# Optimization experiments

Measured on AMD Instinct MI355X. Metric: run time of the kernel, lower is better.

Reference implementation:

```python
import jax, jax.numpy as jnp
import numpy as np

LMAX, MMAX = 4, 2
L = (LMAX + 1) ** 2  # 25 full SH coefficients
_midx = np.concatenate([l * l + l + np.arange(-min(l, MMAX), min(l, MMAX) + 1) for l in range(LMAX + 1)])
M = len(_midx)  # 19 m-restricted coefficients (|m|<=mmax)
_l_of = np.concatenate([np.full(2 * l + 1, l) for l in range(LMAX + 1)])
MIDX = jnp.asarray(_midx)
L_OF = jnp.asarray(_l_of)
LMAP = jnp.asarray((_l_of[:, None] == np.arange(LMAX + 1)[None, :]).astype(np.float32))  # [L, lmax+1]
COUNTS = jnp.asarray((2 * np.arange(LMAX + 1) + 1).astype(np.float32))
AVG_DEGREE = 23.395238876342773
AVG_NUM_NODES = 77.81317
N_NODES, N_EDGES, N_GRAPH = 2500, 50000, 16
C, H, A, VC, FF, NB, NL = 128, 8, 64, 16, 128, 600, 4
MAX_R = 12.0

def rms_norm_sh(x, scale):
    # per-degree-l RMS norm with learned per-(l, channel) scale; x [N,L,C]
    ms = jnp.einsum('nlc,lk->nk', x * x, LMAP) / (COUNTS * x.shape[-1])
    inv = jax.lax.rsqrt(ms + 1e-8)[:, L_OF]  # [N,L]
    return x * inv[..., None] * scale[L_OF][None]

def seg_softmax(logits, seg, n):
    m = jax.ops.segment_max(logits, seg, num_segments=n)
    e = jnp.exp(logits - m[seg])
    s = jax.ops.segment_sum(e, seg, num_segments=n)
    return e / (s[seg] + 1e-9)

def _forward(edge_distance, sphere_emb, W_e1, W_e2, W_deg, norm_scale, norm_scale2,
             Wq, Wk, alpha_vec, Wv, W_rad, Wo, W1, W2, norm_scale_final, W_ef1, W_ef2,
             atomic_numbers, edge_index, batch):
    src, tgt = edge_index[0], edge_index[1]
    # GaussianSmearing(0, max_radius, 600, basis_width_scalar=2.0)
    offset = jnp.linspace(0.0, MAX_R, NB)
    coeff = -0.5 / (2.0 * (MAX_R / (NB - 1))) ** 2
    smear = jnp.exp(coeff * (edge_distance[:, None] - offset[None, :]) ** 2)  # [E,NB]
    efeat = jax.nn.silu(jax.nn.silu(smear @ W_e1) @ W_e2)  # shared radial edge features [E,C]
    # sphere embedding into l=0 coefficient
    x = jnp.zeros((N_NODES, L, C), edge_distance.dtype)
    x = x.at[:, 0, :].set(sphere_emb[atomic_numbers])
    # edge degree embedding: per-edge coefficients scattered to target nodes
    deg = (efeat @ W_deg).reshape(N_EDGES, M, C)
    x = x.at[:, MIDX, :].add(jax.ops.segment_sum(deg, tgt, num_segments=N_NODES) / AVG_DEGREE)
    for i in range(NL):
        # --- SO2 equivariant graph attention ---
        xn = rms_norm_sh(x, norm_scale[i])
        s = xn[:, 0, :]  # invariant (l=0) features [N,C]
        q = (s @ Wq[i]).reshape(N_NODES, H, A)[tgt]
        k = (s @ Wk[i]).reshape(N_NODES, H, A)[src]
        logits = jnp.einsum('eha,ha->eh', jax.nn.silu(q + k), alpha_vec[i]) / np.sqrt(A).astype(np.float32)
        attn = seg_softmax(logits, tgt, N_NODES)  # [E,H]
        rad = jax.nn.silu(efeat @ W_rad[i])  # per-edge per-coefficient radial gate [E,M]
        xm = xn[:, MIDX, :][src] * rad[..., None]  # gather m-restricted coeffs [E,M,C]
        v = jnp.einsum('emc,cd->emd', xm, Wv[i]).reshape(N_EDGES, M, H, VC)
        msg = (v * attn[:, None, :, None]).reshape(N_EDGES, M, H * VC)
        out = jnp.einsum('emd,dc->emc', msg, Wo[i])
        x = x.at[:, MIDX, :].add(jax.ops.segment_sum(out, tgt, num_segments=N_NODES))
        # --- FFN with separable S2 (scalar-gated) activation ---
        xn = rms_norm_sh(x, norm_scale2[i])
        h = jnp.einsum('nlc,cf->nlf', xn, W1[i])
        h = h * jax.nn.silu(h[:, :1, :])
        x = x + jnp.einsum('nlf,fc->nlc', h, W2[i])
    # energy head
    xn = rms_norm_sh(x, norm_scale_final)
    h = jnp.einsum('nlc,cf->nlf', xn, W_ef1)
    h = h * jax.nn.silu(h[:, :1, :])
    node_e = jnp.einsum('nlf,fo->nlo', h, W_ef2)[:, 0, 0]  # l=0 scalar per node
    return jax.ops.segment_sum(node_e, batch, num_segments=N_GRAPH) / AVG_NUM_NODES

def setup_inputs() -> dict:
    key = jax.random.key(0)
    ks = jax.random.split(key, 24)
    rn = lambda k, shp, fan: jax.random.normal(k, shp, jnp.float32) / np.sqrt(fan).astype(np.float32)
    inp = {}
    inp['atomic_numbers'] = jax.random.randint(ks[0], (N_NODES,), 0, 90)
    inp['edge_index'] = jax.random.randint(ks[1], (2, N_EDGES), 0, N_NODES)
    inp['edge_distance'] = jax.random.uniform(ks[2], (N_EDGES,), jnp.float32) * MAX_R
    inp['batch'] = jnp.sort(jax.random.randint(ks[3], (N_NODES,), 0, N_GRAPH))
    inp['sphere_emb'] = rn(ks[4], (90, C), 1)
    inp['W_e1'] = rn(ks[5], (NB, C), NB)
    inp['W_e2'] = rn(ks[6], (C, C), C)
    inp['W_deg'] = rn(ks[7], (C, M * C), C)
    inp['norm_scale'] = jnp.ones((NL, LMAX + 1, C), jnp.float32)
    inp['norm_scale2'] = jnp.ones((NL, LMAX + 1, C), jnp.float32)
    inp['Wq'] = rn(ks[8], (NL, C, H * A), C)
    inp['Wk'] = rn(ks[9], (NL, C, H * A), C)
    inp['alpha_vec'] = rn(ks[10], (NL, H, A), A)
    inp['Wv'] = rn(ks[11], (NL, C, H * VC), C)
    inp['W_rad'] = rn(ks[12], (NL, C, M), C)
    inp['Wo'] = rn(ks[13], (NL, H * VC, C), H * VC)
    inp['W1'] = rn(ks[14], (NL, C, FF), C)
    inp['W2'] = rn(ks[15], (NL, FF, C), FF)
    inp['norm_scale_final'] = jnp.ones((LMAX + 1, C), jnp.float32)
    inp['W_ef1'] = rn(ks[16], (C, FF), C)
    inp['W_ef2'] = rn(ks[17], (FF, 1), FF)
    return inp

def reference(atomic_numbers, edge_index, edge_distance, batch, sphere_emb, W_e1, W_e2, W_deg,
              norm_scale, norm_scale2, Wq, Wk, alpha_vec, Wv, W_rad, Wo, W1, W2,
              norm_scale_final, W_ef1, W_ef2):
    return _forward(edge_distance, sphere_emb, W_e1, W_e2, W_deg, norm_scale, norm_scale2,
                    Wq, Wk, alpha_vec, Wv, W_rad, Wo, W1, W2, norm_scale_final, W_ef1, W_ef2,
                    atomic_numbers, edge_index, batch)
```

## Files before the change

kernel.cpp:

```cpp
#include <hip/hip_runtime.h>
#include <hip/hip_bf16.h>

#define N_NODES 2500
#define N_EDGES 50000
#define C 128
#define MC 19
#define RSTR 20
#define NL 4
#define NB 600
#define GW 12
#define NTAP (2*GW+1)
#define NBUK 4
#define BUKW 625
#define N4 (N_NODES*NBUK)
#define ASTR 136
#define MSTR 132
#define MAXE 96
#define EB 64

typedef float floatx2 __attribute__((ext_vector_type(2)));
typedef short bf16x8 __attribute__((ext_vector_type(8)));
typedef float f32x4 __attribute__((ext_vector_type(4)));

__device__ __forceinline__ float silu(float v){ return v / (1.f + expf(-v)); }
__device__ __forceinline__ int l_of_m(int m){
  return (m==0)?0 : (m<4)?1 : (m<9)?2 : (m<14)?3 : 4;
}
__device__ __forceinline__ unsigned pack2(float a, float b){
  __hip_bfloat162 h2;
  h2.x = __float2bfloat16(a);
  h2.y = __float2bfloat16(b);
  return *(unsigned*)&h2;
}
__device__ __forceinline__ unsigned short bf16of(float v){
  __hip_bfloat16 h = __float2bfloat16(v);
  return *(unsigned short*)&h;
}
__device__ __forceinline__ float2 bf2f2(unsigned u){
  float2 r;
  r.x = __uint_as_float(u << 16);
  r.y = __uint_as_float(u & 0xffff0000u);
  return r;
}
__device__ __forceinline__ bf16x8 packbf8(float4 a, float4 b){
  union { unsigned u[4]; bf16x8 v; } r;
  r.u[0] = pack2(a.x, a.y); r.u[1] = pack2(a.z, a.w);
  r.u[2] = pack2(b.x, b.y); r.u[3] = pack2(b.z, b.w);
  return r.v;
}
__device__ __forceinline__ unsigned short packfp8(float a, float b){
  float ac = fminf(fmaxf(a, -448.f), 448.f);
  float bc = fminf(fmaxf(b, -448.f), 448.f);
  return (unsigned short)((unsigned)__builtin_amdgcn_cvt_pk_fp8_f32(ac, bc, 0, false) & 0xffffu);
}

__global__ __launch_bounds__(256) void k_packall(
    const float* __restrict__ We2, const float* __restrict__ Wv, const float* __restrict__ Wo,
    const float* __restrict__ W1, const float* __restrict__ W2,
    const float* __restrict__ Wq, const float* __restrict__ Wk,
    unsigned short* we2t, unsigned short* wvt, unsigned short* wot,
    unsigned short* w1t, unsigned short* w2t, unsigned short* wqt, unsigned short* wkt){
  unsigned id = blockIdx.x*256 + threadIdx.x;
  const unsigned PERL = 98304u;
  if (id < 8192u){
    unsigned f = id & 127u, cp = id >> 7;
    *(unsigned*)&we2t[f*C + 2*cp] = pack2(We2[(2*cp)*C + f], We2[(2*cp+1)*C + f]);
    return;
  }
  unsigned rem = id - 8192u;
  unsigned layer = rem / PERL;
  if (layer >= 4u) return;
// ... 170 lines not shown
        const float* __restrict__ emb, const int* __restrict__ anum, float* __restrict__ x){
  __shared__ __align__(16) float efT[C][16];
  int t = threadIdx.x;
  int n0 = blockIdx.x*16;
  int grp = blockIdx.y;
  for (int q=t; q<16*C; q+=256){
    int cc=q>>4, nd=q&15;
    int n=n0+nd;
    efT[cc][nd] = (n<N_NODES)? efsumT[(size_t)cc*N_NODES + n] : 0.f;
  }
  __syncthreads();
  const float inv_avg = 1.0f/23.395238876342773f;
  int o = grp*512 + t*2;
  if (o < MC*C){
    float a0[16], a1[16];
    #pragma unroll
    for (int i=0;i<16;i++){ a0[i]=0.f; a1[i]=0.f; }
    for (int cc=0; cc<C; ++cc){
      float2 w = *(const float2*)&Wdeg[(size_t)cc*(MC*C)+o];
      float4 e0 = *(const float4*)&efT[cc][0];
      float4 e1 = *(const float4*)&efT[cc][4];
      float4 e2 = *(const float4*)&efT[cc][8];
      float4 e3 = *(const float4*)&efT[cc][12];
      a0[0]+=e0.x*w.x; a1[0]+=e0.x*w.y;
      a0[1]+=e0.y*w.x; a1[1]+=e0.y*w.y;
      a0[2]+=e0.z*w.x; a1[2]+=e0.z*w.y;
      a0[3]+=e0.w*w.x; a1[3]+=e0.w*w.y;
      a0[4]+=e1.x*w.x; a1[4]+=e1.x*w.y;
      a0[5]+=e1.y*w.x; a1[5]+=e1.y*w.y;
      a0[6]+=e1.z*w.x; a1[6]+=e1.z*w.y;
      a0[7]+=e1.w*w.x; a1[7]+=e1.w*w.y;
      a0[8]+=e2.x*w.x; a1[8]+=e2.x*w.y;
      a0[9]+=e2.y*w.x; a1[9]+=e2.y*w.y;
      a0[10]+=e2.z*w.x; a1[10]+=e2.z*w.y;
      a0[11]+=e2.w*w.x; a1[11]+=e2.w*w.y;
      a0[12]+=e3.x*w.x; a1[12]+=e3.x*w.y;
      a0[13]+=e3.y*w.x; a1[13]+=e3.y*w.y;
      a0[14]+=e3.z*w.x; a1[14]+=e3.z*w.y;
      a0[15]+=e3.w*w.x; a1[15]+=e3.w*w.y;
    }
    #pragma unroll
    for (int nd=0; nd<16; ++nd){
      int n = n0+nd;
      if (n < N_NODES){
        float v0 = a0[nd]*inv_avg, v1 = a1[nd]*inv_avg;
        if (o < C){ int an=anum[n]; v0 += emb[an*C+o]; v1 += emb[an*C+o+1]; }
        float2 st; st.x=v0; st.y=v1;
        *(float2*)&x[(size_t)n*MC*C + o] = st;
      }
    }
  }
}

__global__ __launch_bounds__(256) void k_qk(const float* __restrict__ x, const float* __restrict__ scale0,
        const unsigned short* __restrict__ wqt, const unsigned short* __restrict__ wkt,
        unsigned short* __restrict__ qb, unsigned short* __restrict__ kb){
  __shared__ __align__(16) float sn[32][132];
  __shared__ float ps[32][8];
  __shared__ float invs[32];
  __shared__ __align__(16) unsigned short A16[32*ASTR];
  int t = threadIdx.x;
  int n0 = blockIdx.x*32;
  int grp = blockIdx.y;
  const unsigned short* WTg = (grp < 4) ? wqt : wkt;
  int cb = (grp & 3)*128;
  unsigned short* outb = (grp < 4) ? qb : kb;
  {
    int nd = t>>3, seg = t&7;
    int n = n0+nd;
    float ss = 0.f;
    if (n < N_NODES){
      const float* xr = &x[(size_t)n*MC*C];
      #pragma unroll
      for (int i=0;i<16;i++){
        int c = seg*16+i;
        float v = xr[c];
        ss += v*v;
        sn[nd][c] = v*scale0[c];
      }
    } else {
      #pragma unroll
      for (int i=0;i<16;i++) sn[nd][seg*16+i] = 0.f;
    }
    ps[nd][seg] = ss;
  }
  __syncthreads();
  if (t < 32){
    float s = 0.f;
    #pragma unroll
    for (int i=0;i<8;i++) s += ps[t][i];
    invs[t] = 1.0f/sqrtf(s*(1.0f/128.f) + 1e-8f);
  }
  __syncthreads();
  for (int q=t; q<32*64; q+=256){
    int r = q>>6, c2 = (q&63)*2;
    float inv = invs[r];
    *(unsigned*)&A16[r*ASTR + c2] = pack2(sn[r][c2]*inv, sn[r][c2+1]*inv);
  }
  __syncthreads();
  int w = t>>6, lane = t&63;
  int lr = lane & 15, lg = lane >> 4;
  int colb = 32*w;
  f32x4 acc[2][2];
  #pragma unroll
  for (int rt=0;rt<2;rt++)
    #pragma unroll
    for (int ci=0;ci<2;ci++){ acc[rt][ci][0]=0.f; acc[rt][ci][1]=0.f; acc[rt][ci][2]=0.f; acc[rt][ci][3]=0.f; }
  #pragma unroll
  for (int ks=0; ks<4; ++ks){
    int k0 = ks*32 + lg*8;
    const unsigned short* Ab = &A16[lr*ASTR + k0];
    bf16x8 a0 = *(const bf16x8*)(Ab);
    bf16x8 a1 = *(const bf16x8*)(Ab + 16*ASTR);
    const unsigned short* Bb = &WTg[(size_t)(cb + colb + lr)*C + k0];
    bf16x8 b0 = *(const bf16x8*)(Bb);
    bf16x8 b1 = *(const bf16x8*)(Bb + 16*C);
    acc[0][0] = __builtin_amdgcn_mfma_f32_16x16x32_bf16(a0, b0, acc[0][0], 0, 0, 0);
    acc[1][0] = __builtin_amdgcn_mfma_f32_16x16x32_bf16(a1, b0, acc[1][0], 0, 0, 0);
    acc[0][1] = __builtin_amdgcn_mfma_f32_16x16x32_bf16(a0, b1, acc[0][1], 0, 0, 0);
    acc[1][1] = __builtin_amdgcn_mfma_f32_16x16x32_bf16(a1, b1, acc[1][1], 0, 0, 0);
  }
  #pragma unroll
  for (int rt=0;rt<2;rt++){
    #pragma unroll
    for (int ci=0;ci<2;ci++){
      int col = colb + 16*ci + lr;
      #pragma unroll
      for (int q=0;q<4;q++){
        int r = 16*rt + lg*4 + q;
        int n = n0 + r;
        if (n < N_NODES)
          outb[(size_t)n*512 + cb + col] = bf16of(acc[rt][ci][q]);
      }
    }
  }
}

__global__ __launch_bounds__(256) void k_nodeA(const float* __restrict__ x, const float* __restrict__ scale,
        const unsigned short* __restrict__ wvt, unsigned char* __restrict__ V){
  __shared__ __align__(16) unsigned short A16[80*ASTR];
  int t = threadIdx.x;
  int n0 = blockIdx.x*4;
  int w = t>>6, lane = t&63;
  int lr = lane & 15, lg = lane >> 4;
  {
    int n = n0 + w;
    float2 xv[MC];
    float pl[5]={0.f,0.f,0.f,0.f,0.f};
    #pragma unroll
    for (int m=0;m<MC;m++){
      float2 v = *(const float2*)&x[(size_t)n*MC*C + m*C + lane*2];
      xv[m]=v;
      pl[l_of_m(m)] += v.x*v.x + v.y*v.y;
    }
    #pragma unroll
    for (int l=0;l<5;l++){
      float r = pl[l];
      #pragma unroll
      for (int d=32; d>0; d>>=1) r += __shfl_xor(r, d, 64);
      pl[l]=r;
    }
    const float dens[5] = {128.f,384.f,640.f,896.f,1152.f};
    float inv[5];
    #pragma unroll
    for (int l=0;l<5;l++) inv[l] = 1.0f/sqrtf(pl[l]/dens[l] + 1e-8f);
    #pragma unroll
    for (int m=0;m<MC;m++){
      int l = l_of_m(m);
      float2 sc = *(const float2*)&scale[l*C + lane*2];
      float a = xv[m].x*inv[l]*sc.x, b = xv[m].y*inv[l]*sc.y;
      *(unsigned*)&A16[(w*MC + m)*ASTR + lane*2] = pack2(a, b);
    }
  }
  for (int q=t; q<272; q+=256)
    ((unsigned*)A16)[(76*ASTR)/2 + q] = 0u;
  __syncthreads();
  int colb = 32*w;
  f32x4 acc[5][2];
  #pragma unroll
  for (int rt=0;rt<5;rt++)
    #pragma unroll
    for (int ci=0;ci<2;ci++){ acc[rt][ci][0]=0.f; acc[rt][ci][1]=0.f; acc[rt][ci][2]=0.f; acc[rt][ci][3]=0.f; }
  #pragma unroll
  for (int ks=0; ks<4; ++ks){
    int k0 = ks*32 + lg*8;
    const unsigned short* Ab = &A16[lr*ASTR + k0];
    bf16x8 a0 = *(const bf16x8*)(Ab);
    bf16x8 a1 = *(const bf16x8*)(Ab + 16*ASTR);
    bf16x8 a2 = *(const bf16x8*)(Ab + 32*ASTR);
    bf16x8 a3 = *(const bf16x8*)(Ab + 48*ASTR);
    bf16x8 a4 = *(const bf16x8*)(Ab + 64*ASTR);
    const unsigned short* Bb = &wvt[(colb + lr)*C + k0];
    bf16x8 b0 = *(const bf16x8*)(Bb);
    bf16x8 b1 = *(const bf16x8*)(Bb + 16*C);
    acc[0][0] = __builtin_amdgcn_mfma_f32_16x16x32_bf16(a0, b0, acc[0][0], 0, 0, 0);
    acc[1][0] = __builtin_amdgcn_mfma_f32_16x16x32_bf16(a1, b0, acc[1][0], 0, 0, 0);
    acc[2][0] = __builtin_amdgcn_mfma_f32_16x16x32_bf16(a2, b0, acc[2][0], 0, 0, 0);
    acc[3][0] = __builtin_amdgcn_mfma_f32_16x16x32_bf16(a3, b0, acc[3][0], 0, 0, 0);
    acc[4][0] = __builtin_amdgcn_mfma_f32_16x16x32_bf16(a4, b0, acc[4][0], 0, 0, 0);
    acc[0][1] = __builtin_amdgcn_mfma_f32_16x16x32_bf16(a0, b1, acc[0][1], 0, 0, 0);
    acc[1][1] = __builtin_amdgcn_mfma_f32_16x16x32_bf16(a1, b1, acc[1][1], 0, 0, 0);
    acc[2][1] = __builtin_amdgcn_mfma_f32_16x16x32_bf16(a2, b1, acc[2][1], 0, 0, 0);
    acc[3][1] = __builtin_amdgcn_mfma_f32_16x16x32_bf16(a3, b1, acc[3][1], 0, 0, 0);
    acc[4][1] = __builtin_amdgcn_mfma_f32_16x16x32_bf16(a4, b1, acc[4][1], 0, 0, 0);
  }
  __syncthreads();
  #pragma unroll
  for (int rt=0;rt<5;rt++){
    #pragma unroll
    for (int ci=0;ci<2;ci++){
      int col = colb + 16*ci + lr;
      #pragma unroll
      for (int q=0;q<4;q++){
        int r = 16*rt + lg*4 + q;
        A16[r*ASTR + col] = bf16of(acc[rt][ci][q]);
      }
    }
  }
  __syncthreads();
  for (int q=t; q<76*64; q+=256){
    int r = q>>6;
    int c2 = (q&63)*2;
    unsigned u = *(unsigned*)&A16[r*ASTR + c2];
    float2 f = bf2f2(u);
    *(unsigned short*)&V[((size_t)(n0*MC + r))*C + c2] = packfp8(f.x, f.y);
  }
}

__global__ __launch_bounds__(256) void k_attn(const unsigned short* __restrict__ qb,
        const unsigned short* __restrict__ kb, const float* __restrict__ alpha,
        const int* __restrict__ rowptr, const int2* __restrict__ epair, float* __restrict__ attnb){
  __shared__ float lw[4][MAXE][8];
  __shared__ int eid[4][MAXE];
  int t = threadIdx.x;
  int w = t>>6, lane = t&63;
  int n = blockIdx.x*4 + w;
  float al[8];
  {
    float4 a0 = *(const float4*)&alpha[lane*8];
    float4 a1 = *(const float4*)&alpha[lane*8+4];
    al[0]=a0.x; al[1]=a0.y; al[2]=a0.z; al[3]=a0.w;
    al[4]=a1.x; al[5]=a1.y; al[6]=a1.z; al[7]=a1.w;
  }
  float qf[8];
  {
    int4 qv = *(const int4*)&qb[(size_t)n*512 + lane*8];
    unsigned qu[4] = {(unsigned)qv.x,(unsigned)qv.y,(unsigned)qv.z,(unsigned)qv.w};
    #pragma unroll
    for (int j=0;j<4;j++){
      float2 q2 = bf2f2(qu[j]);
      qf[2*j] = q2.x; qf[2*j+1] = q2.y;
    }
  }
  int beg = rowptr[n*NBUK], end = rowptr[n*NBUK+NBUK];
  int cnt = end - beg; if (cnt > MAXE) cnt = MAXE;
  int i = 0;
  for (; i+2 <= cnt; i += 2){
    int2 p0 = epair[beg+i];
    int2 p1 = epair[beg+i+1];
    int4 kv0 = *(const int4*)&kb[(size_t)p0.y*512 + lane*8];
    int4 kv1 = *(const int4*)&kb[(size_t)p1.y*512 + lane*8];
    unsigned ku0[4] = {(unsigned)kv0.x,(unsigned)kv0.y,(unsigned)kv0.z,(unsigned)kv0.w};
    unsigned ku1[4] = {(unsigned)kv1.x,(unsigned)kv1.y,(unsigned)kv1.z,(unsigned)kv1.w};
    float acc0 = 0.f, acc1 = 0.f;
    #pragma unroll
    for (int j=0;j<4;j++){
      float2 k0 = bf2f2(ku0[j]);
      float2 k1 = bf2f2(ku1[j]);
      acc0 += silu(qf[2*j]+k0.x)*al[2*j] + silu(qf[2*j+1]+k0.y)*al[2*j+1];
      acc1 += silu(qf[2*j]+k1.x)*al[2*j] + silu(qf[2*j+1]+k1.y)*al[2*j+1];
    }
    #pragma unroll
    for (int d=1; d<8; d<<=1){
      acc0 += __shfl_down(acc0, d, 64);
      acc1 += __shfl_down(acc1, d, 64);
    }
    if ((lane&7)==0){
      lw[w][i][lane>>3]   = acc0 * 0.125f;
      lw[w][i+1][lane>>3] = acc1 * 0.125f;
    }
    if (lane==0){ eid[w][i] = p0.x; eid[w][i+1] = p1.x; }
  }
  for (; i < cnt; ++i){
    int2 p0 = epair[beg+i];
    int4 kv0 = *(const int4*)&kb[(size_t)p0.y*512 + lane*8];
    unsigned ku0[4] = {(unsigned)kv0.x,(unsigned)kv0.y,(unsigned)kv0.z,(unsigned)kv0.w};
    float acc0 = 0.f;
    #pragma unroll
    for (int j=0;j<4;j++){
      float2 k0 = bf2f2(ku0[j]);
      acc0 += silu(qf[2*j]+k0.x)*al[2*j] + silu(qf[2*j+1]+k0.y)*al[2*j+1];
    }
    #pragma unroll
    for (int d=1; d<8; d<<=1) acc0 += __shfl_down(acc0, d, 64);
    if ((lane&7)==0) lw[w][i][lane>>3] = acc0 * 0.125f;
    if (lane==0) eid[w][i] = p0.x;
  }
  __syncthreads();
  int h = lane & 7, ec = lane >> 3;
  float mx = -1e30f;
  for (int q=ec; q<cnt; q+=8) mx = fmaxf(mx, lw[w][q][h]);
  #pragma unroll
  for (int dd=8; dd<64; dd<<=1) mx = fmaxf(mx, __shfl_xor(mx, dd, 64));
  float sum = 0.f;
  for (int q=ec; q<cnt; q+=8) sum += expf(lw[w][q][h] - mx);
  #pragma unroll
  for (int dd=8; dd<64; dd<<=1) sum += __shfl_xor(sum, dd, 64);
  float inv = 1.0f/(sum + 1e-9f);
  for (int q=ec; q<cnt; q+=8)
    attnb[eid[w][q]*8 + h] = expf(lw[w][q][h] - mx) * inv;
}

__global__ __launch_bounds__(256) void k_rad(const float* __restrict__ efeat, const float* __restrict__ Wrad,
                                             float* __restrict__ radb){
  __shared__ __align__(16) unsigned short A16[EB*ASTR];
  __shared__ __align__(16) unsigned short WT[32*ASTR];
  int t = threadIdx.x;
  int e0 = blockIdx.x*EB;
  for (int q=t; q<EB*64; q+=256){
    int r = q>>6, c2 = (q&63)*2;
    int e = e0 + r;
    float2 f2;
    if (e < N_EDGES) f2 = *(const float2*)&efeat[(size_t)e*C + c2];
    else { f2.x=0.f; f2.y=0.f; }
    *(unsigned*)&A16[r*ASTR + c2] = pack2(f2.x, f2.y);
  }
  for (int q=t; q<32*64; q+=256){
    int m = q>>6, c2 = (q&63)*2;
    float w0 = (m < MC) ? Wrad[(size_t)c2*MC + m] : 0.f;
    float w1 = (m < MC) ? Wrad[(size_t)(c2+1)*MC + m] : 0.f;
    *(unsigned*)&WT[m*ASTR + c2] = pack2(w0, w1);
  }
  __syncthreads();
  int w = t>>6, lane = t&63;
  int lr = lane & 15, lg = lane >> 4;
  f32x4 acc[2];
  acc[0][0]=0.f; acc[0][1]=0.f; acc[0][2]=0.f; acc[0][3]=0.f;
  acc[1][0]=0.f; acc[1][1]=0.f; acc[1][2]=0.f; acc[1][3]=0.f;
  #pragma unroll
  for (int ks=0; ks<4; ++ks){
    int k0 = ks*32 + lg*8;
    bf16x8 a  = *(const bf16x8*)&A16[(16*w + lr)*ASTR + k0];
    bf16x8 b0 = *(const bf16x8*)&WT[lr*ASTR + k0];
    bf16x8 b1 = *(const bf16x8*)&WT[(16+lr)*ASTR + k0];
    acc[0] = __builtin_amdgcn_mfma_f32_16x16x32_bf16(a, b0, acc[0], 0, 0, 0);
    acc[1] = __builtin_amdgcn_mfma_f32_16x16x32_bf16(a, b1, acc[1], 0, 0, 0);
  }
  #pragma unroll
  for (int ci=0;ci<2;ci++){
    int m = 16*ci + lr;
    #pragma unroll
    for (int q=0;q<4;q++){
      int r = 16*w + lg*4 + q;
      int e = e0 + r;
      if (m < MC && e < N_EDGES)
        radb[(size_t)e*RSTR + m] = silu(acc[ci][q]);
    }
  }
}

#define CONS1(vv, ar)  { \
    floatx2 g0 = __builtin_amdgcn_cvt_pk_f32_fp8((vv).x, false); \
    floatx2 g1 = __builtin_amdgcn_cvt_pk_f32_fp8((vv).x, true);  \
    floatx2 g2 = __builtin_amdgcn_cvt_pk_f32_fp8((vv).y, false); \
    floatx2 g3 = __builtin_amdgcn_cvt_pk_f32_fp8((vv).y, true);  \
    acc1[0] += (ar)*g0[0]; acc1[1] += (ar)*g0[1]; \
    acc1[2] += (ar)*g1[0]; acc1[3] += (ar)*g1[1]; \
    acc1[4] += (ar)*g2[0]; acc1[5] += (ar)*g2[1]; \
    acc1[6] += (ar)*g3[0]; acc1[7] += (ar)*g3[1]; }
#define CONS2(vv, ar)  { \
    floatx2 g0 = __builtin_amdgcn_cvt_pk_f32_fp8((vv).x, false); \
    floatx2 g1 = __builtin_amdgcn_cvt_pk_f32_fp8((vv).x, true);  \
    floatx2 g2 = __builtin_amdgcn_cvt_pk_f32_fp8((vv).y, false); \
    floatx2 g3 = __builtin_amdgcn_cvt_pk_f32_fp8((vv).y, true);  \
    acc2[0] += (ar)*g0[0]; acc2[1] += (ar)*g0[1]; \
    acc2[2] += (ar)*g1[0]; acc2[3] += (ar)*g1[1]; \
    acc2[4] += (ar)*g2[0]; acc2[5] += (ar)*g2[1]; \
    acc2[6] += (ar)*g3[0]; acc2[7] += (ar)*g3[1]; }
__global__ __launch_bounds__(256, 4) void k_e1(const unsigned char* __restrict__ V, const float* __restrict__ radb,
        const float* __restrict__ attnb, const unsigned short* __restrict__ wot,
        const int* __restrict__ rowptr, const int2* __restrict__ epair,
        float* __restrict__ x){
  __shared__ __align__(16) float msum[32*MSTR];
  int n = blockIdx.x;
  int t = threadIdx.x;
  int w = t>>6, lane = t&63;
  for (int q=t; q<13*MSTR; q+=256) msum[19*MSTR + q] = 0.f;
  int chunk = lane & 15;
  int g = lane >> 4;
  int m1 = w*5 + g;
  int c1 = chunk*8;
  int h1 = chunk>>1;
  int m2 = w*5 + 4;
  bool has2 = (w < 3) && (lane < 16);
  int voff1 = m1*C + c1;
  int voff2 = m2*C + lane*8;
  int h2 = lane>>1;
  float acc1[8], acc2[8];
  #pragma unroll
  for (int j=0;j<8;j++){ acc1[j]=0.f; acc2[j]=0.f; }
  int beg = rowptr[n*NBUK], end = rowptr[n*NBUK+NBUK];
  int idx = beg;
  for (; idx+4 <= end; idx += 4){
    int2 p0 = epair[idx];
    int2 p1 = epair[idx+1];
    int2 p2 = epair[idx+2];
    int2 p3 = epair[idx+3];
    const unsigned char* vb0 = V + (size_t)p0.y*(MC*C);
    const unsigned char* vb1 = V + (size_t)p1.y*(MC*C);
// ... 281 lines not shown
  const float* emb   = (const float*)d_in[4];
  const float* We1   = (const float*)d_in[5];
  const float* We2   = (const float*)d_in[6];
  const float* Wdeg  = (const float*)d_in[7];
  const float* ns1   = (const float*)d_in[8];
  const float* ns2   = (const float*)d_in[9];
  const float* Wq    = (const float*)d_in[10];
  const float* Wk    = (const float*)d_in[11];
  const float* alpha = (const float*)d_in[12];
  const float* Wv    = (const float*)d_in[13];
  const float* Wrad  = (const float*)d_in[14];
  const float* Wo    = (const float*)d_in[15];
  const float* W1    = (const float*)d_in[16];
  const float* W2    = (const float*)d_in[17];
  const float* nsf   = (const float*)d_in[18];
  const float* Wef1  = (const float*)d_in[19];
  const float* Wef2  = (const float*)d_in[20];
  float* out = (float*)d_out;

  const int* srcarr = eidx;
  const int* tgtarr = eidx + N_EDGES;

  char* wsb = (char*)d_ws;
  float* efeat = (float*)wsb;  wsb += (size_t)N_EDGES*C*4;
  float* efsumT= (float*)wsb;  wsb += (size_t)N_NODES*C*4;
  float* x     = (float*)wsb;  wsb += (size_t)N_NODES*MC*C*4;
  unsigned char* Vb = (unsigned char*)wsb; wsb += (size_t)N_NODES*MC*C;
  unsigned short* qb = (unsigned short*)wsb; wsb += (size_t)N_NODES*512*2;
  unsigned short* kb = (unsigned short*)wsb; wsb += (size_t)N_NODES*512*2;
  float* attnb = (float*)wsb;  wsb += (size_t)N_EDGES*8*4;
  float* radb  = (float*)wsb;  wsb += (size_t)N_EDGES*RSTR*4;
  int* deg     = (int*)wsb;    wsb += (size_t)N4*4;
  int* rowptr  = (int*)wsb;    wsb += (size_t)(N4+1)*4;
  int* cursor  = (int*)wsb;    wsb += (size_t)N4*4;
  int* elist   = (int*)wsb;    wsb += (size_t)N_EDGES*4;
  int2* epair  = (int2*)wsb;   wsb += (size_t)N_EDGES*8;
  unsigned short* we2t = (unsigned short*)wsb; wsb += (size_t)16384*2;
  unsigned short* wvt  = (unsigned short*)wsb; wsb += (size_t)4*16384*2;
  unsigned short* wot  = (unsigned short*)wsb; wsb += (size_t)4*16384*2;
  unsigned short* w1t  = (unsigned short*)wsb; wsb += (size_t)4*16384*2;
  unsigned short* w2t  = (unsigned short*)wsb; wsb += (size_t)4*16384*2;
  unsigned short* wqt  = (unsigned short*)wsb; wsb += (size_t)4*65536*2;
  unsigned short* wkt  = (unsigned short*)wsb; wsb += (size_t)4*65536*2;

  (void)hipMemsetAsync(deg, 0, N4*4, stream);
  (void)hipMemsetAsync(cursor, 0, N4*4, stream);
  (void)hipMemsetAsync(d_out, 0, (size_t)out_size*sizeof(float), stream);

  k_packall<<<1568, 256, 0, stream>>>(We2, Wv, Wo, W1, W2, Wq, Wk,
                                      we2t, wvt, wot, w1t, w2t, wqt, wkt);
  k_count<<<(N_EDGES+255)/256, 256, 0, stream>>>(tgtarr, srcarr, deg);
  k_scan<<<1, 1024, 0, stream>>>(deg, rowptr);
  k_fill<<<(N_EDGES+255)/256, 256, 0, stream>>>(tgtarr, srcarr, rowptr, cursor, elist, epair);
  k_efeat<<<(N_EDGES+EB-1)/EB, 256, 0, stream>>>(dist, We1, we2t, efeat);
  k_efsum<<<N_NODES, 128, 0, stream>>>(efeat, rowptr, elist, efsumT);
  k_deginit<<<dim3((N_NODES+15)/16, 5), 256, 0, stream>>>(efsumT, Wdeg, emb, anum, x);

  for (int i=0;i<NL;i++){
    k_nodeA<<<N_NODES/4, 256, 0, stream>>>(x, ns1 + i*5*C, wvt + (size_t)i*16384, Vb);
    k_qk<<<dim3((N_NODES+31)/32, 8), 256, 0, stream>>>(x, ns1 + i*5*C,
                                                       wqt + (size_t)i*65536, wkt + (size_t)i*65536,
                                                       qb, kb);
    k_attn<<<N_NODES/4, 256, 0, stream>>>(qb, kb, alpha + i*512, rowptr, epair, attnb);
    k_rad<<<(N_EDGES+EB-1)/EB, 256, 0, stream>>>(efeat, Wrad + i*C*MC, radb);
    k_e1<<<N_NODES, 256, 0, stream>>>(Vb, radb, attnb, wot + (size_t)i*16384,
                                      rowptr, epair, x);
    k_nodeB<<<N_NODES/2/2, 256, 0, stream>>>(x, ns2 + i*5*C, w1t + (size_t)i*16384, w2t + (size_t)i*16384);
  }
  k_final<<<N_NODES, 128, 0, stream>>>(x, nsf, Wef1, Wef2, batch, out);
}
```

Baseline: 753.0 us.

## Merge independent per-layer kernels into horizontally fused launches

Within each layer, the value-projection kernel and the Q/K projection kernel now run as one launch, with block index deciding which branch runs, and the shared memory is carved from one byte buffer. The attention-softmax kernel and the radial-weight kernel are combined the same way. This removes two launches per layer and lets independent work fill the GPU at the same time, at the cost of the larger shared memory footprint and register pressure of the heavier branch applying to every block. It also narrows the Gaussian tap window constant GW from 12 to 10, which changes how many smearing taps are kept.

```diff
diff --git a/kernel.cpp b/kernel.cpp
--- a/kernel.cpp
+++ b/kernel.cpp
@@ -8,7 +8,7 @@
 #define RSTR 20
 #define NL 4
 #define NB 600
-#define GW 12
+#define GW 10
 #define NTAP (2*GW+1)
 #define NBUK 4
 #define BUKW 625
@@ -17,6 +17,8 @@
 #define MSTR 132
 #define MAXE 96
 #define EB 64
+#define NQKB ((N_NODES+31)/32)
+#define NRADB ((N_EDGES+EB-1)/EB)
 
 typedef float floatx2 __attribute__((ext_vector_type(2)));
 typedef short bf16x8 __attribute__((ext_vector_type(8)));
@@ -293,309 +295,307 @@
   }
 }
 
-__global__ __launch_bounds__(256) void k_qk(const float* __restrict__ x, const float* __restrict__ scale0,
-        const unsigned short* __restrict__ wqt, const unsigned short* __restrict__ wkt,
-        unsigned short* __restrict__ qb, unsigned short* __restrict__ kb){
-  __shared__ __align__(16) float sn[32][132];
-  __shared__ float ps[32][8];
-  __shared__ float invs[32];
-  __shared__ __align__(16) unsigned short A16[32*ASTR];
+__global__ __launch_bounds__(256) void k_nAqk(const float* __restrict__ x, const float* __restrict__ scale0,
+        const unsigned short* __restrict__ wvt, const unsigned short* __restrict__ wqt,
+        const unsigned short* __restrict__ wkt,
+        unsigned char* __restrict__ V, unsigned short* __restrict__ qb, unsigned short* __restrict__ kb){
+  __shared__ __align__(16) char smem[26880];
   int t = threadIdx.x;
-  int n0 = blockIdx.x*32;
-  int grp = blockIdx.y;
-  const unsigned short* WTg = (grp < 4) ? wqt : wkt;
-  int cb = (grp & 3)*128;
-  unsigned short* outb = (grp < 4) ? qb : kb;
-  {
-    int nd = t>>3, seg = t&7;
-    int n = n0+nd;
-    float ss = 0.f;
-    if (n < N_NODES){
-      const float* xr = &x[(size_t)n*MC*C];
-      #pragma unroll
-      for (int i=0;i<16;i++){
-        int c = seg*16+i;
-        float v = xr[c];
-        ss += v*v;
-        sn[nd][c] = v*scale0[c];
-      }
-    } else {
-      #pragma unroll
-      for (int i=0;i<16;i++) sn[nd][seg*16+i] = 0.f;
-    }
-    ps[nd][seg] = ss;
-  }
-  __syncthreads();
-  if (t < 32){
-    float s = 0.f;
-    #pragma unroll
-    for (int i=0;i<8;i++) s += ps[t][i];
-    invs[t] = 1.0f/sqrtf(s*(1.0f/128.f) + 1e-8f);
-  }
-  __syncthreads();
-  for (int q=t; q<32*64; q+=256){
-    int r = q>>6, c2 = (q&63)*2;
-    float inv = invs[r];
-    *(unsigned*)&A16[r*ASTR + c2] = pack2(sn[r][c2]*inv, sn[r][c2+1]*inv);
-  }
-  __syncthreads();
   int w = t>>6, lane = t&63;
   int lr = lane & 15, lg = lane >> 4;
-  int colb = 32*w;
-  f32x4 acc[2][2];
-  #pragma unroll
-  for (int rt=0;rt<2;rt++)
-    #pragma unroll
-    for (int ci=0;ci<2;ci++){ acc[rt][ci][0]=0.f; acc[rt][ci][1]=0.f; acc[rt][ci][2]=0.f; acc[rt][ci][3]=0.f; }
-  #pragma unroll
-  for (int ks=0; ks<4; ++ks){
-    int k0 = ks*32 + lg*8;
-    const unsigned short* Ab = &A16[lr*ASTR + k0];
-    bf16x8 a0 = *(const bf16x8*)(Ab);
-    bf16x8 a1 = *(const bf16x8*)(Ab + 16*ASTR);
-    const unsigned short* Bb = &WTg[(size_t)(cb + colb + lr)*C + k0];
-    bf16x8 b0 = *(const bf16x8*)(Bb);
-    bf16x8 b1 = *(const bf16x8*)(Bb + 16*C);
-    acc[0][0] = __builtin_amdgcn_mfma_f32_16x16x32_bf16(a0, b0, acc[0][0], 0, 0, 0);
-    acc[1][0] = __builtin_amdgcn_mfma_f32_16x16x32_bf16(a1, b0, acc[1][0], 0, 0, 0);
-    acc[0][1] = __builtin_amdgcn_mfma_f32_16x16x32_bf16(a0, b1, acc[0][1], 0, 0, 0);
-    acc[1][1] = __builtin_amdgcn_mfma_f32_16x16x32_bf16(a1, b1, acc[1][1], 0, 0, 0);
-  }
-  #pragma unroll
-  for (int rt=0;rt<2;rt++){
-    #pragma unroll
-    for (int ci=0;ci<2;ci++){
-      int col = colb + 16*ci + lr;
-      #pragma unroll
-      for (int q=0;q<4;q++){
-        int r = 16*rt + lg*4 + q;
-        int n = n0 + r;
-        if (n < N_NODES)
-          outb[(size_t)n*512 + cb + col] = bf16of(acc[rt][ci][q]);
-      }
-    }
-  }
-}
-
-__global__ __launch_bounds__(256) void k_nodeA(const float* __restrict__ x, const float* __restrict__ scale,
-        const unsigned short* __restrict__ wvt, unsigned char* __restrict__ V){
-  __shared__ __align__(16) unsigned short A16[80*ASTR];
-  int t = threadIdx.x;
-  int n0 = blockIdx.x*4;
-  int w = t>>6, lane = t&63;
-  int lr = lane & 15, lg = lane >> 4;
-  {
-    int n = n0 + w;
-    float2 xv[MC];
-    float pl[5]={0.f,0.f,0.f,0.f,0.f};
-    #pragma unroll
-    for (int m=0;m<MC;m++){
-      float2 v = *(const float2*)&x[(size_t)n*MC*C + m*C + lane*2];
-      xv[m]=v;
-      pl[l_of_m(m)] += v.x*v.x + v.y*v.y;
-    }
-    #pragma unroll
-    for (int l=0;l<5;l++){
-      float r = pl[l];
-      #pragma unroll
-      for (int d=32; d>0; d>>=1) r += __shfl_xor(r, d, 64);
-      pl[l]=r;
-    }
-    const float dens[5] = {128.f,384.f,640.f,896.f,1152.f};
-    float inv[5];
-    #pragma unroll
-    for (int l=0;l<5;l++) inv[l] = 1.0f/sqrtf(pl[l]/dens[l] + 1e-8f);
-    #pragma unroll
-    for (int m=0;m<MC;m++){
-      int l = l_of_m(m);
-      float2 sc = *(const float2*)&scale[l*C + lane*2];
-      float a = xv[m].x*inv[l]*sc.x, b = xv[m].y*inv[l]*sc.y;
-      *(unsigned*)&A16[(w*MC + m)*ASTR + lane*2] = pack2(a, b);
-    }
-  }
-  for (int q=t; q<272; q+=256)
-    ((unsigned*)A16)[(76*ASTR)/2 + q] = 0u;
-  __syncthreads();
-  int colb = 32*w;
-  f32x4 acc[5][2];
-  #pragma unroll
-  for (int rt=0;rt<5;rt++)
-    #pragma unroll
-    for (int ci=0;ci<2;ci++){ acc[rt][ci][0]=0.f; acc[rt][ci][1]=0.f; acc[rt][ci][2]=0.f; acc[rt][ci][3]=0.f; }
-  #pragma unroll
-  for (int ks=0; ks<4; ++ks){
-    int k0 = ks*32 + lg*8;
-    const unsigned short* Ab = &A16[lr*ASTR + k0];
-    bf16x8 a0 = *(const bf16x8*)(Ab);
-    bf16x8 a1 = *(const bf16x8*)(Ab + 16*ASTR);
-    bf16x8 a2 = *(const bf16x8*)(Ab + 32*ASTR);
-    bf16x8 a3 = *(const bf16x8*)(Ab + 48*ASTR);
-    bf16x8 a4 = *(const bf16x8*)(Ab + 64*ASTR);
-    const unsigned short* Bb = &wvt[(colb + lr)*C + k0];
-    bf16x8 b0 = *(const bf16x8*)(Bb);
-    bf16x8 b1 = *(const bf16x8*)(Bb + 16*C);
-    acc[0][0] = __builtin_amdgcn_mfma_f32_16x16x32_bf16(a0, b0, acc[0][0], 0, 0, 0);
-    acc[1][0] = __builtin_amdgcn_mfma_f32_16x16x32_bf16(a1, b0, acc[1][0], 0, 0, 0);
-    acc[2][0] = __builtin_amdgcn_mfma_f32_16x16x32_bf16(a2, b0, acc[2][0], 0, 0, 0);
-    acc[3][0] = __builtin_amdgcn_mfma_f32_16x16x32_bf16(a3, b0, acc[3][0], 0, 0, 0);
-    acc[4][0] = __builtin_amdgcn_mfma_f32_16x16x32_bf16(a4, b0, acc[4][0], 0, 0, 0);
-    acc[0][1] = __builtin_amdgcn_mfma_f32_16x16x32_bf16(a0, b1, acc[0][1], 0, 0, 0);
-    acc[1][1] = __builtin_amdgcn_mfma_f32_16x16x32_bf16(a1, b1, acc[1][1], 0, 0, 0);
-    acc[2][1] = __builtin_amdgcn_mfma_f32_16x16x32_bf16(a2, b1, acc[2][1], 0, 0, 0);
-    acc[3][1] = __builtin_amdgcn_mfma_f32_16x16x32_bf16(a3, b1, acc[3][1], 0, 0, 0);
-    acc[4][1] = __builtin_amdgcn_mfma_f32_16x16x32_bf16(a4, b1, acc[4][1], 0, 0, 0);
-  }
-  __syncthreads();
-  #pragma unroll
-  for (int rt=0;rt<5;rt++){
-    #pragma unroll
-    for (int ci=0;ci<2;ci++){
-      int col = colb + 16*ci + lr;
-      #pragma unroll
-      for (int q=0;q<4;q++){
-        int r = 16*rt + lg*4 + q;
-        A16[r*ASTR + col] = bf16of(acc[rt][ci][q]);
-      }
-    }
-  }
-  __syncthreads();
-  for (int q=t; q<76*64; q+=256){
-    int r = q>>6;
-    int c2 = (q&63)*2;
-    unsigned u = *(unsigned*)&A16[r*ASTR + c2];
-    float2 f = bf2f2(u);
-    *(unsigned short*)&V[((size_t)(n0*MC + r))*C + c2] = packfp8(f.x, f.y);
-  }
-}
-
-__global__ __launch_bounds__(256) void k_attn(const unsigned short* __restrict__ qb,
+  if (blockIdx.x < (unsigned)(N_NODES/4)){
+    unsigned short* A16 = (unsigned short*)smem;
+    int n0 = blockIdx.x*4;
+    {
+      int n = n0 + w;
+      float2 xv[MC];
+      float pl[5]={0.f,0.f,0.f,0.f,0.f};
+      #pragma unroll
+      for (int m=0;m<MC;m++){
+        float2 v = *(const float2*)&x[(size_t)n*MC*C + m*C + lane*2];
+        xv[m]=v;
+        pl[l_of_m(m)] += v.x*v.x + v.y*v.y;
+      }
+      #pragma unroll
+      for (int l=0;l<5;l++){
+        float r = pl[l];
+        #pragma unroll
+        for (int d=32; d>0; d>>=1) r += __shfl_xor(r, d, 64);
+        pl[l]=r;
+      }
+      const float dens[5] = {128.f,384.f,640.f,896.f,1152.f};
+      float inv[5];
+      #pragma unroll
+      for (int l=0;l<5;l++) inv[l] = 1.0f/sqrtf(pl[l]/dens[l] + 1e-8f);
+      #pragma unroll
+      for (int m=0;m<MC;m++){
+        int l = l_of_m(m);
+        float2 sc = *(const float2*)&scale0[l*C + lane*2];
+        float a = xv[m].x*inv[l]*sc.x, b = xv[m].y*inv[l]*sc.y;
+        *(unsigned*)&A16[(w*MC + m)*ASTR + lane*2] = pack2(a, b);
+      }
+    }
+    for (int q=t; q<272; q+=256)
+      ((unsigned*)A16)[(76*ASTR)/2 + q] = 0u;
+    __syncthreads();
+    int colb = 32*w;
+    f32x4 acc[5][2];
+    #pragma unroll
+    for (int rt=0;rt<5;rt++)
+      #pragma unroll
+      for (int ci=0;ci<2;ci++){ acc[rt][ci][0]=0.f; acc[rt][ci][1]=0.f; acc[rt][ci][2]=0.f; acc[rt][ci][3]=0.f; }
+    #pragma unroll
+    for (int ks=0; ks<4; ++ks){
+      int k0 = ks*32 + lg*8;
+      const unsigned short* Ab = &A16[lr*ASTR + k0];
+      bf16x8 a0 = *(const bf16x8*)(Ab);
+      bf16x8 a1 = *(const bf16x8*)(Ab + 16*ASTR);
+      bf16x8 a2 = *(const bf16x8*)(Ab + 32*ASTR);
+      bf16x8 a3 = *(const bf16x8*)(Ab + 48*ASTR);
+      bf16x8 a4 = *(const bf16x8*)(Ab + 64*ASTR);
+      const unsigned short* Bb = &wvt[(colb + lr)*C + k0];
+      bf16x8 b0 = *(const bf16x8*)(Bb);
+      bf16x8 b1 = *(const bf16x8*)(Bb + 16*C);
+      acc[0][0] = __builtin_amdgcn_mfma_f32_16x16x32_bf16(a0, b0, acc[0][0], 0, 0, 0);
+      acc[1][0] = __builtin_amdgcn_mfma_f32_16x16x32_bf16(a1, b0, acc[1][0], 0, 0, 0);
+      acc[2][0] = __builtin_amdgcn_mfma_f32_16x16x32_bf16(a2, b0, acc[2][0], 0, 0, 0);
+      acc[3][0] = __builtin_amdgcn_mfma_f32_16x16x32_bf16(a3, b0, acc[3][0], 0, 0, 0);
+      acc[4][0] = __builtin_amdgcn_mfma_f32_16x16x32_bf16(a4, b0, acc[4][0], 0, 0, 0);
+      acc[0][1] = __builtin_amdgcn_mfma_f32_16x16x32_bf16(a0, b1, acc[0][1], 0, 0, 0);
+      acc[1][1] = __builtin_amdgcn_mfma_f32_16x16x32_bf16(a1, b1, acc[1][1], 0, 0, 0);
+      acc[2][1] = __builtin_amdgcn_mfma_f32_16x16x32_bf16(a2, b1, acc[2][1], 0, 0, 0);
+      acc[3][1] = __builtin_amdgcn_mfma_f32_16x16x32_bf16(a3, b1, acc[3][1], 0, 0, 0);
+      acc[4][1] = __builtin_amdgcn_mfma_f32_16x16x32_bf16(a4, b1, acc[4][1], 0, 0, 0);
+    }
+    __syncthreads();
+    #pragma unroll
+    for (int rt=0;rt<5;rt++){
+      #pragma unroll
+      for (int ci=0;ci<2;ci++){
+        int col = colb + 16*ci + lr;
+        #pragma unroll
+        for (int q=0;q<4;q++){
+          int r = 16*rt + lg*4 + q;
+          A16[r*ASTR + col] = bf16of(acc[rt][ci][q]);
+        }
+      }
+    }
+    __syncthreads();
+    for (int q=t; q<76*64; q+=256){
+      int r = q>>6;
+      int c2 = (q&63)*2;
+      unsigned u = *(unsigned*)&A16[r*ASTR + c2];
+      float2 f = bf2f2(u);
+      *(unsigned short*)&V[((size_t)(n0*MC + r))*C + c2] = packfp8(f.x, f.y);
+    }
+  } else {
+    int qq = blockIdx.x - N_NODES/4;
+    int grp = qq / NQKB;
+    int n0 = (qq - grp*NQKB)*32;
+    float (*sn)[132] = (float(*)[132])smem;
+    float (*ps)[8] = (float(*)[8])(smem + 16896);
+    float* invs = (float*)(smem + 16896 + 1024);
+    unsigned short* A16 = (unsigned short*)(smem + 16896 + 1024 + 128);
+    const unsigned short* WTg = (grp < 4) ? wqt : wkt;
+    int cb = (grp & 3)*128;
+    unsigned short* outb = (grp < 4) ? qb : kb;
+    {
+      int nd = t>>3, seg = t&7;
+      int n = n0+nd;
+      float ss = 0.f;
+      if (n < N_NODES){
+        const float* xr = &x[(size_t)n*MC*C];
+        #pragma unroll
+        for (int i=0;i<16;i++){
+          int c = seg*16+i;
+          float v = xr[c];
+          ss += v*v;
+          sn[nd][c] = v*scale0[c];
+        }
+      } else {
+        #pragma unroll
+        for (int i=0;i<16;i++) sn[nd][seg*16+i] = 0.f;
+      }
+      ps[nd][seg] = ss;
+    }
+    __syncthreads();
+    if (t < 32){
+      float s = 0.f;
+      #pragma unroll
+      for (int i=0;i<8;i++) s += ps[t][i];
+      invs[t] = 1.0f/sqrtf(s*(1.0f/128.f) + 1e-8f);
+    }
+    __syncthreads();
+    for (int q=t; q<32*64; q+=256){
+      int r = q>>6, c2 = (q&63)*2;
+      float inv = invs[r];
+      *(unsigned*)&A16[r*ASTR + c2] = pack2(sn[r][c2]*inv, sn[r][c2+1]*inv);
+    }
+    __syncthreads();
+    int colb = 32*w;
+    f32x4 acc[2][2];
+    #pragma unroll
+    for (int rt=0;rt<2;rt++)
+      #pragma unroll
+      for (int ci=0;ci<2;ci++){ acc[rt][ci][0]=0.f; acc[rt][ci][1]=0.f; acc[rt][ci][2]=0.f; acc[rt][ci][3]=0.f; }
+    #pragma unroll
+    for (int ks=0; ks<4; ++ks){
+      int k0 = ks*32 + lg*8;
+      const unsigned short* Ab = &A16[lr*ASTR + k0];
+      bf16x8 a0 = *(const bf16x8*)(Ab);
+      bf16x8 a1 = *(const bf16x8*)(Ab + 16*ASTR);
+      const unsigned short* Bb = &WTg[(size_t)(cb + colb + lr)*C + k0];
+      bf16x8 b0 = *(const bf16x8*)(Bb);
+      bf16x8 b1 = *(const bf16x8*)(Bb + 16*C);
+      acc[0][0] = __builtin_amdgcn_mfma_f32_16x16x32_bf16(a0, b0, acc[0][0], 0, 0, 0);
+      acc[1][0] = __builtin_amdgcn_mfma_f32_16x16x32_bf16(a1, b0, acc[1][0], 0, 0, 0);
+      acc[0][1] = __builtin_amdgcn_mfma_f32_16x16x32_bf16(a0, b1, acc[0][1], 0, 0, 0);
+      acc[1][1] = __builtin_amdgcn_mfma_f32_16x16x32_bf16(a1, b1, acc[1][1], 0, 0, 0);
+    }
+    #pragma unroll
+    for (int rt=0;rt<2;rt++){
+      #pragma unroll
+      for (int ci=0;ci<2;ci++){
+        int col = colb + 16*ci + lr;
+        #pragma unroll
+        for (int q=0;q<4;q++){
+          int r = 16*rt + lg*4 + q;
+          int n = n0 + r;
+          if (n < N_NODES)
+            outb[(size_t)n*512 + cb + col] = bf16of(acc[rt][ci][q]);
+        }
+      }
+    }
+  }
+}
+
+__global__ __launch_bounds__(256) void k_attnrad(const unsigned short* __restrict__ qb,
         const unsigned short* __restrict__ kb, const float* __restrict__ alpha,
-        const int* __restrict__ rowptr, const int2* __restrict__ epair, float* __restrict__ attnb){
-  __shared__ float lw[4][MAXE][8];
-  __shared__ int eid[4][MAXE];
+        const int* __restrict__ rowptr, const int2* __restrict__ epair, float* __restrict__ attnb,
+        const float* __restrict__ efeat, const float* __restrict__ Wrad, float* __restrict__ radb){
+  __shared__ __align__(16) char smem[26112];
   int t = threadIdx.x;
   int w = t>>6, lane = t&63;
-  int n = blockIdx.x*4 + w;
-  float al[8];
-  {
-    float4 a0 = *(const float4*)&alpha[lane*8];
-    float4 a1 = *(const float4*)&alpha[lane*8+4];
-    al[0]=a0.x; al[1]=a0.y; al[2]=a0.z; al[3]=a0.w;
-    al[4]=a1.x; al[5]=a1.y; al[6]=a1.z; al[7]=a1.w;
-  }
-  float qf[8];
-  {
-    int4 qv = *(const int4*)&qb[(size_t)n*512 + lane*8];
-    unsigned qu[4] = {(unsigned)qv.x,(unsigned)qv.y,(unsigned)qv.z,(unsigned)qv.w};
-    #pragma unroll
-    for (int j=0;j<4;j++){
-      float2 q2 = bf2f2(qu[j]);
-      qf[2*j] = q2.x; qf[2*j+1] = q2.y;
-    }
-  }
-  int beg = rowptr[n*NBUK], end = rowptr[n*NBUK+NBUK];
-  int cnt = end - beg; if (cnt > MAXE) cnt = MAXE;
-  int i = 0;
-  for (; i+2 <= cnt; i += 2){
-    int2 p0 = epair[beg+i];
-    int2 p1 = epair[beg+i+1];
-    int4 kv0 = *(const int4*)&kb[(size_t)p0.y*512 + lane*8];
-    int4 kv1 = *(const int4*)&kb[(size_t)p1.y*512 + lane*8];
-    unsigned ku0[4] = {(unsigned)kv0.x,(unsigned)kv0.y,(unsigned)kv0.z,(unsigned)kv0.w};
-    unsigned ku1[4] = {(unsigned)kv1.x,(unsigned)kv1.y,(unsigned)kv1.z,(unsigned)kv1.w};
-    float acc0 = 0.f, acc1 = 0.f;
-    #pragma unroll
-    for (int j=0;j<4;j++){
-      float2 k0 = bf2f2(ku0[j]);
-      float2 k1 = bf2f2(ku1[j]);
-      acc0 += silu(qf[2*j]+k0.x)*al[2*j] + silu(qf[2*j+1]+k0.y)*al[2*j+1];
-      acc1 += silu(qf[2*j]+k1.x)*al[2*j] + silu(qf[2*j+1]+k1.y)*al[2*j+1];
-    }
-    #pragma unroll
-    for (int d=1; d<8; d<<=1){
-      acc0 += __shfl_down(acc0, d, 64);
-      acc1 += __shfl_down(acc1, d, 64);
-    }
-    if ((lane&7)==0){
-      lw[w][i][lane>>3]   = acc0 * 0.125f;
-      lw[w][i+1][lane>>3] = acc1 * 0.125f;
-    }
-    if (lane==0){ eid[w][i] = p0.x; eid[w][i+1] = p1.x; }
-  }
-  for (; i < cnt; ++i){
-    int2 p0 = epair[beg+i];
-    int4 kv0 = *(const int4*)&kb[(size_t)p0.y*512 + lane*8];
-    unsigned ku0[4] = {(unsigned)kv0.x,(unsigned)kv0.y,(unsigned)kv0.z,(unsigned)kv0.w};
-    float acc0 = 0.f;
-    #pragma unroll
-    for (int j=0;j<4;j++){
-      float2 k0 = bf2f2(ku0[j]);
-      acc0 += silu(qf[2*j]+k0.x)*al[2*j] + silu(qf[2*j+1]+k0.y)*al[2*j+1];
-    }
-    #pragma unroll
-    for (int d=1; d<8; d<<=1) acc0 += __shfl_down(acc0, d, 64);
-    if ((lane&7)==0) lw[w][i][lane>>3] = acc0 * 0.125f;
-    if (lane==0) eid[w][i] = p0.x;
-  }
-  __syncthreads();
-  int h = lane & 7, ec = lane >> 3;
-  float mx = -1e30f;
-  for (int q=ec; q<cnt; q+=8) mx = fmaxf(mx, lw[w][q][h]);
-  #pragma unroll
-  for (int dd=8; dd<64; dd<<=1) mx = fmaxf(mx, __shfl_xor(mx, dd, 64));
-  float sum = 0.f;
-  for (int q=ec; q<cnt; q+=8) sum += expf(lw[w][q][h] - mx);
-  #pragma unroll
-  for (int dd=8; dd<64; dd<<=1) sum += __shfl_xor(sum, dd, 64);
-  float inv = 1.0f/(sum + 1e-9f);
-  for (int q=ec; q<cnt; q+=8)
-    attnb[eid[w][q]*8 + h] = expf(lw[w][q][h] - mx) * inv;
-}
-
-__global__ __launch_bounds__(256) void k_rad(const float* __restrict__ efeat, const float* __restrict__ Wrad,
-                                             float* __restrict__ radb){
-  __shared__ __align__(16) unsigned short A16[EB*ASTR];
-  __shared__ __align__(16) unsigned short WT[32*ASTR];
-  int t = threadIdx.x;
-  int e0 = blockIdx.x*EB;
-  for (int q=t; q<EB*64; q+=256){
-    int r = q>>6, c2 = (q&63)*2;
-    int e = e0 + r;
-    float2 f2;
-    if (e < N_EDGES) f2 = *(const float2*)&efeat[(size_t)e*C + c2];
-    else { f2.x=0.f; f2.y=0.f; }
-    *(unsigned*)&A16[r*ASTR + c2] = pack2(f2.x, f2.y);
-  }
-  for (int q=t; q<32*64; q+=256){
-    int m = q>>6, c2 = (q&63)*2;
-    float w0 = (m < MC) ? Wrad[(size_t)c2*MC + m] : 0.f;
-    float w1 = (m < MC) ? Wrad[(size_t)(c2+1)*MC + m] : 0.f;
-    *(unsigned*)&WT[m*ASTR + c2] = pack2(w0, w1);
-  }
-  __syncthreads();
-  int w = t>>6, lane = t&63;
-  int lr = lane & 15, lg = lane >> 4;
-  f32x4 acc[2];
-  acc[0][0]=0.f; acc[0][1]=0.f; acc[0][2]=0.f; acc[0][3]=0.f;
-  acc[1][0]=0.f; acc[1][1]=0.f; acc[1][2]=0.f; acc[1][3]=0.f;
-  #pragma unroll
-  for (int ks=0; ks<4; ++ks){
-    int k0 = ks*32 + lg*8;
-    bf16x8 a  = *(const bf16x8*)&A16[(16*w + lr)*ASTR + k0];
-    bf16x8 b0 = *(const bf16x8*)&WT[lr*ASTR + k0];
-    bf16x8 b1 = *(const bf16x8*)&WT[(16+lr)*ASTR + k0];
-    acc[0] = __builtin_amdgcn_mfma_f32_16x16x32_bf16(a, b0, acc[0], 0, 0, 0);
-    acc[1] = __builtin_amdgcn_mfma_f32_16x16x32_bf16(a, b1, acc[1], 0, 0, 0);
-  }
-  #pragma unroll
-  for (int ci=0;ci<2;ci++){
-    int m = 16*ci + lr;
-    #pragma unroll
-    for (int q=0;q<4;q++){
-      int r = 16*w + lg*4 + q;
+  if (blockIdx.x < (unsigned)(N_NODES/4)){
+    float (*lw)[MAXE][8] = (float(*)[MAXE][8])smem;
+    int (*eid)[MAXE] = (int(*)[MAXE])(smem + 12288);
+    int n = blockIdx.x*4 + w;
+    float al[8];
+    {
+      float4 a0 = *(const float4*)&alpha[lane*8];
+      float4 a1 = *(const float4*)&alpha[lane*8+4];
+      al[0]=a0.x; al[1]=a0.y; al[2]=a0.z; al[3]=a0.w;
+      al[4]=a1.x; al[5]=a1.y; al[6]=a1.z; al[7]=a1.w;
+    }
+    float qf[8];
+    {
+      int4 qv = *(const int4*)&qb[(size_t)n*512 + lane*8];
+      unsigned qu[4] = {(unsigned)qv.x,(unsigned)qv.y,(unsigned)qv.z,(unsigned)qv.w};
+      #pragma unroll
+      for (int j=0;j<4;j++){
+        float2 q2 = bf2f2(qu[j]);
+        qf[2*j] = q2.x; qf[2*j+1] = q2.y;
+      }
+    }
+    int beg = rowptr[n*NBUK], end = rowptr[n*NBUK+NBUK];
+    int cnt = end - beg; if (cnt > MAXE) cnt = MAXE;
+    int i = 0;
+    for (; i+2 <= cnt; i += 2){
+      int2 p0 = epair[beg+i];
+      int2 p1 = epair[beg+i+1];
+      int4 kv0 = *(const int4*)&kb[(size_t)p0.y*512 + lane*8];
+      int4 kv1 = *(const int4*)&kb[(size_t)p1.y*512 + lane*8];
+      unsigned ku0[4] = {(unsigned)kv0.x,(unsigned)kv0.y,(unsigned)kv0.z,(unsigned)kv0.w};
+      unsigned ku1[4] = {(unsigned)kv1.x,(unsigned)kv1.y,(unsigned)kv1.z,(unsigned)kv1.w};
+      float acc0 = 0.f, acc1 = 0.f;
+      #pragma unroll
+      for (int j=0;j<4;j++){
+        float2 k0 = bf2f2(ku0[j]);
+        float2 k1 = bf2f2(ku1[j]);
+        acc0 += silu(qf[2*j]+k0.x)*al[2*j] + silu(qf[2*j+1]+k0.y)*al[2*j+1];
+        acc1 += silu(qf[2*j]+k1.x)*al[2*j] + silu(qf[2*j+1]+k1.y)*al[2*j+1];
+      }
+      #pragma unroll
+      for (int d=1; d<8; d<<=1){
+        acc0 += __shfl_down(acc0, d, 64);
+        acc1 += __shfl_down(acc1, d, 64);
+      }
+      if ((lane&7)==0){
+        lw[w][i][lane>>3]   = acc0 * 0.125f;
+        lw[w][i+1][lane>>3] = acc1 * 0.125f;
+      }
+      if (lane==0){ eid[w][i] = p0.x; eid[w][i+1] = p1.x; }
+    }
+    for (; i < cnt; ++i){
+      int2 p0 = epair[beg+i];
+      int4 kv0 = *(const int4*)&kb[(size_t)p0.y*512 + lane*8];
+      unsigned ku0[4] = {(unsigned)kv0.x,(unsigned)kv0.y,(unsigned)kv0.z,(unsigned)kv0.w};
+      float acc0 = 0.f;
+      #pragma unroll
+      for (int j=0;j<4;j++){
+        float2 k0 = bf2f2(ku0[j]);
+        acc0 += silu(qf[2*j]+k0.x)*al[2*j] + silu(qf[2*j+1]+k0.y)*al[2*j+1];
+      }
+      #pragma unroll
+      for (int d=1; d<8; d<<=1) acc0 += __shfl_down(acc0, d, 64);
+      if ((lane&7)==0) lw[w][i][lane>>3] = acc0 * 0.125f;
+      if (lane==0) eid[w][i] = p0.x;
+    }
+    __syncthreads();
+    int h = lane & 7, ec = lane >> 3;
+    float mx = -1e30f;
+    for (int q=ec; q<cnt; q+=8) mx = fmaxf(mx, lw[w][q][h]);
+    #pragma unroll
+    for (int dd=8; dd<64; dd<<=1) mx = fmaxf(mx, __shfl_xor(mx, dd, 64));
+    float sum = 0.f;
+    for (int q=ec; q<cnt; q+=8) sum += expf(lw[w][q][h] - mx);
+    #pragma unroll
+    for (int dd=8; dd<64; dd<<=1) sum += __shfl_xor(sum, dd, 64);
+    float inv = 1.0f/(sum + 1e-9f);
+    for (int q=ec; q<cnt; q+=8)
+      attnb[eid[w][q]*8 + h] = expf(lw[w][q][h] - mx) * inv;
+  } else {
+    unsigned short* A16 = (unsigned short*)smem;
+    unsigned short* WT = (unsigned short*)(smem + EB*ASTR*2);
+    int e0 = (blockIdx.x - N_NODES/4)*EB;
+    for (int q=t; q<EB*64; q+=256){
+      int r = q>>6, c2 = (q&63)*2;
       int e = e0 + r;
-      if (m < MC && e < N_EDGES)
-        radb[(size_t)e*RSTR + m] = silu(acc[ci][q]);
+      float2 f2;
+      if (e < N_EDGES) f2 = *(const float2*)&efeat[(size_t)e*C + c2];
+      else { f2.x=0.f; f2.y=0.f; }
+      *(unsigned*)&A16[r*ASTR + c2] = pack2(f2.x, f2.y);
+    }
+    for (int q=t; q<32*64; q+=256){
+      int m = q>>6, c2 = (q&63)*2;
+      float w0 = (m < MC) ? Wrad[(size_t)c2*MC + m] : 0.f;
+      float w1 = (m < MC) ? Wrad[(size_t)(c2+1)*MC + m] : 0.f;
+      *(unsigned*)&WT[m*ASTR + c2] = pack2(w0, w1);
+    }
+    __syncthreads();
+    int lr = lane & 15, lg = lane >> 4;
+    f32x4 acc[2];
+    acc[0][0]=0.f; acc[0][1]=0.f; acc[0][2]=0.f; acc[0][3]=0.f;
+    acc[1][0]=0.f; acc[1][1]=0.f; acc[1][2]=0.f; acc[1][3]=0.f;
+    #pragma unroll
+    for (int ks=0; ks<4; ++ks){
+      int k0 = ks*32 + lg*8;
+      bf16x8 a  = *(const bf16x8*)&A16[(16*w + lr)*ASTR + k0];
+      bf16x8 b0 = *(const bf16x8*)&WT[lr*ASTR + k0];
+      bf16x8 b1 = *(const bf16x8*)&WT[(16+lr)*ASTR + k0];
+      acc[0] = __builtin_amdgcn_mfma_f32_16x16x32_bf16(a, b0, acc[0], 0, 0, 0);
+      acc[1] = __builtin_amdgcn_mfma_f32_16x16x32_bf16(a, b1, acc[1], 0, 0, 0);
+    }
+    #pragma unroll
+    for (int ci=0;ci<2;ci++){
+      int m = 16*ci + lr;
+      #pragma unroll
+      for (int q=0;q<4;q++){
+        int r = 16*w + lg*4 + q;
+        int e = e0 + r;
+        if (m < MC && e < N_EDGES)
+          radb[(size_t)e*RSTR + m] = silu(acc[ci][q]);
+      }
     }
   }
 }
@@ -983,20 +983,20 @@
   k_count<<<(N_EDGES+255)/256, 256, 0, stream>>>(tgtarr, srcarr, deg);
   k_scan<<<1, 1024, 0, stream>>>(deg, rowptr);
   k_fill<<<(N_EDGES+255)/256, 256, 0, stream>>>(tgtarr, srcarr, rowptr, cursor, elist, epair);
-  k_efeat<<<(N_EDGES+EB-1)/EB, 256, 0, stream>>>(dist, We1, we2t, efeat);
+  k_efeat<<<NRADB, 256, 0, stream>>>(dist, We1, we2t, efeat);
   k_efsum<<<N_NODES, 128, 0, stream>>>(efeat, rowptr, elist, efsumT);
   k_deginit<<<dim3((N_NODES+15)/16, 5), 256, 0, stream>>>(efsumT, Wdeg, emb, anum, x);
 
   for (int i=0;i<NL;i++){
-    k_nodeA<<<N_NODES/4, 256, 0, stream>>>(x, ns1 + i*5*C, wvt + (size_t)i*16384, Vb);
-    k_qk<<<dim3((N_NODES+31)/32, 8), 256, 0, stream>>>(x, ns1 + i*5*C,
-                                                       wqt + (size_t)i*65536, wkt + (size_t)i*65536,
-                                                       qb, kb);
-    k_attn<<<N_NODES/4, 256, 0, stream>>>(qb, kb, alpha + i*512, rowptr, epair, attnb);
-    k_rad<<<(N_EDGES+EB-1)/EB, 256, 0, stream>>>(efeat, Wrad + i*C*MC, radb);
+    k_nAqk<<<N_NODES/4 + NQKB*8, 256, 0, stream>>>(x, ns1 + i*5*C,
+                                                   wvt + (size_t)i*16384,
+                                                   wqt + (size_t)i*65536, wkt + (size_t)i*65536,
+                                                   Vb, qb, kb);
+    k_attnrad<<<N_NODES/4 + NRADB, 256, 0, stream>>>(qb, kb, alpha + i*512, rowptr, epair, attnb,
+                                                     efeat, Wrad + i*C*MC, radb);
     k_e1<<<N_NODES, 256, 0, stream>>>(Vb, radb, attnb, wot + (size_t)i*16384,
                                       rowptr, epair, x);
-    k_nodeB<<<N_NODES/2/2, 256, 0, stream>>>(x, ns2 + i*5*C, w1t + (size_t)i*16384, w2t + (size_t)i*16384);
+    k_nodeB<<<N_NODES/4, 256, 0, stream>>>(x, ns2 + i*5*C, w1t + (size_t)i*16384, w2t + (size_t)i*16384);
   }
   k_final<<<N_NODES, 128, 0, stream>>>(x, nsf, Wef1, Wef2, batch, out);
 }
```

Measured after the change: 689.4 us. -8.4%, faster.
